# Performance work log

Measured on AMD Instinct MI355X. Metric: run time of the kernel, lower is better.

## Reference

```python
import jax, jax.numpy as jnp
import numpy as np

N = 100000   # nodes
E = 800000   # edges (avg degree 8)
D = 128      # input_dim == output_dim
H = 4        # num_heads
DH = D // H  # head_dim = 32


def setup_inputs() -> dict:
    key = jax.random.key(0)
    ks = jax.random.split(key, 12)
    s = 1.0 / np.sqrt(D)
    x = jax.random.normal(ks[0], (N, D), jnp.float32)
    row = jnp.sort(jax.random.randint(ks[1], (E,), 0, N))  # destination (query) nodes
    col = jax.random.randint(ks[2], (E,), 0, N)            # source (key/value) nodes
    Wq = jax.random.normal(ks[3], (D, D), jnp.float32) * s
    bq = jax.random.normal(ks[4], (D,), jnp.float32) * 0.01
    Wk = jax.random.normal(ks[5], (D, D), jnp.float32) * s
    bk = jax.random.normal(ks[6], (D,), jnp.float32) * 0.01
    Wv = jax.random.normal(ks[7], (D, D), jnp.float32) * s
    bv = jax.random.normal(ks[8], (D,), jnp.float32) * 0.01
    Wo = jax.random.normal(ks[9], (D, D), jnp.float32) * s
    bo = jax.random.normal(ks[10], (D,), jnp.float32) * 0.01
    return {"x": x, "row": row, "col": col, "Wq": Wq, "bq": bq, "Wk": Wk,
            "bk": bk, "Wv": Wv, "bv": bv, "Wo": Wo, "bo": bo}


def reference(x, row, col, Wq, bq, Wk, bk, Wv, bv, Wo, bo):
    n = x.shape[0]
    # projections; reshape (N, head_dim, num_heads) exactly as the torch code
    # NOTE: source scales q by k.size(-1)**0.5 == sqrt(num_heads) (quirk, kept faithful)
    scale = jnp.asarray(H, x.dtype) ** 0.5
    q = ((x @ Wq.T + bq).reshape(n, DH, H)) / scale
    k = (x @ Wk.T + bk).reshape(n, DH, H)
    v = (x @ Wv.T + bv).reshape(n, DH, H)
    # bsddmm: per-edge, per-head scores s[e,h] = q[row[e],:,h] . k[col[e],:,h]
    s = jnp.einsum('edh,edh->eh', q[row], k[col])  # (E, H)
    # sparse row-wise softmax over incoming edges of each destination node
    m = jax.ops.segment_max(s, row, num_segments=n)      # (N, H)
    e = jnp.exp(s - m[row])                               # (E, H)
    z = jax.ops.segment_sum(e, row, num_segments=n)      # (N, H)
    a = e / z[row]                                        # (E, H) attention weights
    # bspmm: y[i,:,h] = sum_{e: row[e]=i} a[e,h] * v[col[e],:,h]
    y = jax.ops.segment_sum(a[:, None, :] * v[col], row, num_segments=n)  # (N, DH, H)
    return y.reshape(n, D) @ Wo.T + bo
```

## Files before the change

kernel.cpp:

```cpp
#include <hip/hip_runtime.h>
#include <hip/hip_bf16.h>
#include <hip/hip_fp16.h>
#include <math.h>

#define D 128
#define H 4

typedef __attribute__((ext_vector_type(8))) short bf16x8;
typedef __attribute__((ext_vector_type(4))) float f32x4;

__device__ __forceinline__ unsigned short f32_to_bf16_rne(float f) {
    union { float f; unsigned u; } c; c.f = f;
    unsigned u = c.u;
    return (unsigned short)((u + 0x7FFFu + ((u >> 16) & 1u)) >> 16);
}
__device__ __forceinline__ float bf16_to_f32(unsigned short h) {
    union { unsigned u; float f; } c; c.u = ((unsigned)h) << 16;
    return c.f;
}

__device__ __forceinline__ void split_store(const float4 f0, const float4 f1,
                                            unsigned short* dh, unsigned short* dl)
{
    float fa[8] = {f0.x, f0.y, f0.z, f0.w, f1.x, f1.y, f1.z, f1.w};
    union { bf16x8 v; unsigned short s[8]; } hv, lv;
#pragma unroll
    for (int j = 0; j < 8; ++j) {
        unsigned short hh = f32_to_bf16_rne(fa[j]);
        hv.s[j] = hh;
        lv.s[j] = f32_to_bf16_rne(fa[j] - bf16_to_f32(hh));
    }
    *(bf16x8*)dh = hv.v;
    *(bf16x8*)dl = lv.v;
}

__global__ __launch_bounds__(256) void convert_w(
    const float* __restrict__ Wq, const float* __restrict__ Wk,
    const float* __restrict__ Wv, const float* __restrict__ Wo,
    unsigned short* __restrict__ wh, unsigned short* __restrict__ wl)
{
    int i = blockIdx.x * blockDim.x + threadIdx.x;
    if (i >= D * D) return;
    int r = i >> 7;
    int c = i & 127;
    int pr = ((r & 3) << 5) | (r >> 2);
    int pc = ((c & 3) << 5) | (c >> 2);
    const float* Ws[4] = {Wq, Wk, Wv, Wo};
#pragma unroll
    for (int m = 0; m < 4; ++m) {
        float f = Ws[m][i];
        unsigned short h = f32_to_bf16_rne(f);
        unsigned short l = f32_to_bf16_rne(f - bf16_to_f32(h));
        int dst = (m < 3) ? (pr * D + c) : (r * D + pc);
        wh[m * D * D + dst] = h;
        wl[m * D * D + dst] = l;
    }
}

#define RT 64

__global__ __launch_bounds__(512) void gemm_pipe(
    const float* __restrict__ A,
    const unsigned short* __restrict__ whAll, const unsigned short* __restrict__ wlAll,
    const float* __restrict__ b0, const float* __restrict__ b1,
    const float* __restrict__ b2,
    void* __restrict__ o0, void* __restrict__ o1, void* __restrict__ o2,
    float scale0, int n, int wbase, int halfmask, int permBias,
    int nsel, int gx)
{
    __shared__ unsigned short Ah[2][RT * 128];
    __shared__ unsigned short Al[2][RT * 128];

    const int sel    = blockIdx.x % nsel;
    const int tile0  = blockIdx.x / nsel;
    const int tstride = gridDim.x / nsel;

    const unsigned short* wh = whAll + (size_t)(wbase + sel) * D * D;
    const unsigned short* wl = wlAll + (size_t)(wbase + sel) * D * D;
    const float* bias = (sel == 0) ? b0 : (sel == 1 ? b1 : b2);
    void* out        = (sel == 0) ? o0 : (sel == 1 ? o1 : o2);
    const float scale = (sel == 0) ? scale0 : 1.0f;
    const bool halfOut = (halfmask >> sel) & 1;

    const int wid  = threadIdx.x >> 6;
    const int lane = threadIdx.x & 63;
    const int quad = lane >> 4;
    const int l16  = lane & 15;

    const unsigned short* wrh = wh + (size_t)(wid * 16 + l16) * D + quad * 8;
    const unsigned short* wrl = wl + (size_t)(wid * 16 + l16) * D + quad * 8;
    bf16x8 bh[4], bl[4];
#pragma unroll
    for (int kc = 0; kc < 4; ++kc) {
        bh[kc] = *(const bf16x8*)(wrh + kc * 32);
        bl[kc] = *(const bf16x8*)(wrl + kc * 32);
    }

    const int idxA = threadIdx.x;
    const int idxB = threadIdx.x + 512;
    const int rA = idxA >> 4, cA = idxA & 15;
    const int rB = idxB >> 4, cB = idxB & 15;
    const int dA = rA * 128 + ((cA ^ (rA & 15)) * 8);
    const int dB = rB * 128 + ((cB ^ (rB & 15)) * 8);

    {
        int rgA = tile0 * RT + rA; if (rgA > n - 1) rgA = n - 1;
        int rgB = tile0 * RT + rB; if (rgB > n - 1) rgB = n - 1;
        const float4* pA = (const float4*)(A + (size_t)rgA * D + cA * 8);
        const float4* pB = (const float4*)(A + (size_t)rgB * D + cB * 8);
        float4 a0 = pA[0], a1 = pA[1], a2 = pB[0], a3 = pB[1];
        split_store(a0, a1, &Ah[0][dA], &Al[0][dA]);
        split_store(a2, a3, &Ah[0][dB], &Al[0][dB]);
    }
    __syncthreads();

    int cur = 0;
    for (int t = tile0; t < gx; t += tstride) {
        const int tn = t + tstride;
        const bool more = (tn < gx);

        float4 a0, a1, a2, a3;
        if (more) {
            int rgA = tn * RT + rA; if (rgA > n - 1) rgA = n - 1;
            int rgB = tn * RT + rB; if (rgB > n - 1) rgB = n - 1;
            const float4* pA = (const float4*)(A + (size_t)rgA * D + cA * 8);
            const float4* pB = (const float4*)(A + (size_t)rgB * D + cB * 8);
            a0 = pA[0]; a1 = pA[1]; a2 = pB[0]; a3 = pB[1];
        }

        f32x4 acc[4];
#pragma unroll
        for (int rt = 0; rt < 4; ++rt) acc[rt] = (f32x4){0.f, 0.f, 0.f, 0.f};

#pragma unroll
        for (int kc = 0; kc < 4; ++kc) {
            const int cs = ((quad + 4 * kc) ^ l16) * 8;
            bf16x8 ah[4], al[4];
#pragma unroll
            for (int rt = 0; rt < 4; ++rt) {
                const int r = rt * 16 + l16;
                ah[rt] = *(const bf16x8*)&Ah[cur][r * 128 + cs];
                al[rt] = *(const bf16x8*)&Al[cur][r * 128 + cs];
            }
#pragma unroll
            for (int rt = 0; rt < 4; ++rt)
                acc[rt] = __builtin_amdgcn_mfma_f32_16x16x32_bf16(ah[rt], bh[kc], acc[rt], 0, 0, 0);
#pragma unroll
            for (int rt = 0; rt < 4; ++rt)
                acc[rt] = __builtin_amdgcn_mfma_f32_16x16x32_bf16(al[rt], bh[kc], acc[rt], 0, 0, 0);
#pragma unroll
            for (int rt = 0; rt < 4; ++rt)
                acc[rt] = __builtin_amdgcn_mfma_f32_16x16x32_bf16(ah[rt], bl[kc], acc[rt], 0, 0, 0);
        }

        const int m0 = t * RT;
        const int colg = wid * 16 + l16;
        const int bidx = permBias ? (((colg & 31) << 2) | (colg >> 5)) : colg;
        const float bv = bias[bidx];
        if (halfOut) {
            __half* oph = (__half*)out;
#pragma unroll
            for (int rt = 0; rt < 4; ++rt) {
#pragma unroll
                for (int r = 0; r < 4; ++r) {
                    int rowg = m0 + rt * 16 + quad * 4 + r;
                    if (rowg < n)
                        oph[(size_t)rowg * D + colg] = __float2half(acc[rt][r] + bv);
                }
            }
        } else {
            float* opf = (float*)out;
#pragma unroll
            for (int rt = 0; rt < 4; ++rt) {
#pragma unroll
                for (int r = 0; r < 4; ++r) {
                    int rowg = m0 + rt * 16 + quad * 4 + r;
                    if (rowg < n)
                        opf[(size_t)rowg * D + colg] = (acc[rt][r] + bv) * scale;
                }
            }
        }

        if (more) {
            split_store(a0, a1, &Ah[cur ^ 1][dA], &Al[cur ^ 1][dA]);
            split_store(a2, a3, &Ah[cur ^ 1][dB], &Al[cur ^ 1][dB]);
        }
        __syncthreads();
        cur ^= 1;
    }
}

__global__ void build_row_start(const int* __restrict__ row,
                                int* __restrict__ row_start, int n, int e)
{
    int i = blockIdx.x * blockDim.x + threadIdx.x;
    if (i > n) return;
    int lo = 0, hi = e;
    while (lo < hi) {
        int mid = (lo + hi) >> 1;
        if (row[mid] < i) lo = mid + 1; else hi = mid;
    }
    row_start[i] = lo;
}

#define MAXDEG 64
#define WPB 4

template<bool BIG>
__device__ __forceinline__ void edge_loop(
    int lane, int sub, int grp, int deg, int e0,
    const int* cmrow, const int* __restrict__ col,
    const float4 qa, const float4 qb,
    const __half* __restrict__ k, const __half* __restrict__ v,
    float& acc0, float& acc1, float& z)
{
    for (int e = 0; e < deg; e += 4) {
        const int ei = e + grp;
        int c0, c1, c2, c3, cs;
        if (!BIG) {
            const int4 cc = *(const int4*)&cmrow[e];
            c0 = cc.x; c1 = cc.y; c2 = cc.z; c3 = cc.w;
            cs = cmrow[ei < deg ? ei : deg - 1];
        } else {
            int es = ei < deg ? ei : deg - 1;
            cs = col[e0 + es];
            int e1 = e + 1 < deg ? e + 1 : deg - 1;
            int e2 = e + 2 < deg ? e + 2 : deg - 1;
            int e3 = e + 3 < deg ? e + 3 : deg - 1;
            c0 = col[e0 + e];
            c1 = col[e0 + e1];
            c2 = col[e0 + e2];
            c3 = col[e0 + e3];
        }
        __half2 v0 = ((const __half2*)(v + ((size_t)c0 << 7)))[lane];
        __half2 v1 = ((const __half2*)(v + ((size_t)c1 << 7)))[lane];
        __half2 v2 = ((const __half2*)(v + ((size_t)c2 << 7)))[lane];
        __half2 v3 = ((const __half2*)(v + ((size_t)c3 << 7)))[lane];
        union { bf16x8 v8; __half hx[8]; } ku;
        ku.v8 = *(const bf16x8*)(k + ((size_t)cs << 7) + sub * 8);
        float p = qa.x * __half2float(ku.hx[0]) + qa.y * __half2float(ku.hx[1])
                + qa.z * __half2float(ku.hx[2]) + qa.w * __half2float(ku.hx[3])
                + qb.x * __half2float(ku.hx[4]) + qb.y * __half2float(ku.hx[5])
                + qb.z * __half2float(ku.hx[6]) + qb.w * __half2float(ku.hx[7]);
        p += __shfl_xor(p, 1);
        p += __shfl_xor(p, 2);
        float ep = (ei < deg) ? __expf(p) : 0.f;
        float a0 = __shfl(ep,      4 * grp);
        float a1 = __shfl(ep, 16 + 4 * grp);
        float a2 = __shfl(ep, 32 + 4 * grp);
        float a3 = __shfl(ep, 48 + 4 * grp);
        z += (a0 + a1) + (a2 + a3);
        acc0 += a0 * __half2float(v0.x) + a1 * __half2float(v1.x)
              + a2 * __half2float(v2.x) + a3 * __half2float(v3.x);
        acc1 += a0 * __half2float(v0.y) + a1 * __half2float(v1.y)
              + a2 * __half2float(v2.y) + a3 * __half2float(v3.y);
    }
}

__global__ __launch_bounds__(WPB * 64) void edge_attn(
    const int* __restrict__ row_start,
    const float* __restrict__ q, const __half* __restrict__ k,
    const __half* __restrict__ v, const int* __restrict__ col,
    float* __restrict__ y, int n)
{
    __shared__ int cm[WPB][MAXDEG];

    const int wid  = threadIdx.x >> 6;
    const int lane = threadIdx.x & 63;
    const int node = blockIdx.x * WPB + wid;
    if (node >= n) return;

    const int e0  = row_start[node];
    const int deg = row_start[node + 1] - e0;
    const int sub = lane & 15;
    const int grp = lane >> 4;

    const float4* q4 = (const float4*)(q + (size_t)node * D) + sub * 2;
    const float4 qa = q4[0], qb = q4[1];

    float acc0 = 0.f, acc1 = 0.f, z = 0.f;

    if (deg <= MAXDEG) {
        const int dl4 = (deg + 3) & ~3;
        for (int i = lane; i < dl4; i += 64) {
            int ii = i < deg ? i : deg - 1;
            cm[wid][i] = col[e0 + ii];
        }
        edge_loop<false>(lane, sub, grp, deg, e0, cm[wid], col, qa, qb, k, v,
                         acc0, acc1, z);
    } else {
        edge_loop<true>(lane, sub, grp, deg, e0, cm[wid], col, qa, qb, k, v,
                        acc0, acc1, z);
    }

    const float rz = (z > 0.f) ? 1.f / z : 0.f;
    acc0 *= rz;
    acc1 *= rz;

    float2 o; o.x = acc0; o.y = acc1;
    ((float2*)y)[(size_t)node * 64 + lane] = o;
}

extern "C" void kernel_launch(void* const* d_in, const int* in_sizes, int n_in,
                              void* d_out, int out_size, void* d_ws, size_t ws_size,
                              hipStream_t stream)
{
    const float* x   = (const float*)d_in[0];
    const int*   row = (const int*)  d_in[1];
    const int*   col = (const int*)  d_in[2];
    const float* Wq  = (const float*)d_in[3];
    const float* bq  = (const float*)d_in[4];
    const float* Wk  = (const float*)d_in[5];
    const float* bk  = (const float*)d_in[6];
    const float* Wv  = (const float*)d_in[7];
    const float* bv  = (const float*)d_in[8];
    const float* Wo  = (const float*)d_in[9];
    const float* bo  = (const float*)d_in[10];
    float* out = (float*)d_out;

    const int n = in_sizes[0] / D;
    const int e = in_sizes[1];
    const size_t ND = (size_t)n * D;

    float* ws = (float*)d_ws;
    float*  q  = ws;
    __half* kh = (__half*)(ws + ND);
    __half* vh = kh + ND;
    float*  y  = ws + 2 * ND;
    unsigned short* wh = (unsigned short*)(ws + 3 * ND);
    unsigned short* wl = wh + 4 * D * D;
    int* row_start = (int*)(wl + 4 * D * D);

    const int gx = (n + RT - 1) / RT;

    convert_w<<<(D * D + 255) / 256, 256, 0, stream>>>(Wq, Wk, Wv, Wo, wh, wl);

    gemm_pipe<<<510, 512, 0, stream>>>(
        x, wh, wl, bq, bk, bv,
        (void*)q, (void*)kh, (void*)vh, 0.5f, n, 0, 6, 1,
        3, gx);

    build_row_start<<<(n + 1 + 255) / 256, 256, 0, stream>>>(row, row_start, n, e);

    edge_attn<<<(n + WPB - 1) / WPB, WPB * 64, 0, stream>>>(
        row_start, q, kh, vh, col, y, n);

    gemm_pipe<<<512, 512, 0, stream>>>(
        y, wh, wl, bo, bo, bo,
        (void*)out, (void*)out, (void*)out, 1.0f, n, 3, 0, 0,
        1, gx);
}
```

Measured before the change: 261.3 us.

## Fuse edge attention with output projection via per-block LDS tile and MFMA

Edge attention and the output projection now run in one kernel. Each 256-thread block processes 32 nodes, four waves of eight nodes each, and stages the attention outputs in shared memory. It then multiplies that tile by Wo with split-bf16 MFMA (hi*hi + lo*hi + hi*lo) and adds the bias. This removes the y intermediate round-trip through global memory and one kernel launch. The cost is that each block reloads Wo slices from global or L2, and occupancy may drop because each wave handles eight nodes serially.

```diff
diff --git a/kernel.cpp b/kernel.cpp
--- a/kernel.cpp
+++ b/kernel.cpp
@@ -19,8 +19,8 @@
     return c.f;
 }
 
-__device__ __forceinline__ void split_store(const float4 f0, const float4 f1,
-                                            unsigned short* dh, unsigned short* dl)
+__device__ __forceinline__ void split8(const float4 f0, const float4 f1,
+                                       bf16x8& hout, bf16x8& lout)
 {
     float fa[8] = {f0.x, f0.y, f0.z, f0.w, f1.x, f1.y, f1.z, f1.w};
     union { bf16x8 v; unsigned short s[8]; } hv, lv;
@@ -30,8 +30,17 @@
         hv.s[j] = hh;
         lv.s[j] = f32_to_bf16_rne(fa[j] - bf16_to_f32(hh));
     }
-    *(bf16x8*)dh = hv.v;
-    *(bf16x8*)dl = lv.v;
+    hout = hv.v;
+    lout = lv.v;
+}
+
+__device__ __forceinline__ void split_store(const float4 f0, const float4 f1,
+                                            unsigned short* dh, unsigned short* dl)
+{
+    bf16x8 h, l;
+    split8(f0, f1, h, l);
+    *(bf16x8*)dh = h;
+    *(bf16x8*)dl = l;
 }
 
 __global__ __launch_bounds__(256) void convert_w(
@@ -204,7 +213,8 @@
 }
 
 #define MAXDEG 64
-#define WPB 4
+#define NPB 32
+#define YLD 132
 
 template<bool BIG>
 __device__ __forceinline__ void edge_loop(
@@ -257,48 +267,99 @@
     }
 }
 
-__global__ __launch_bounds__(WPB * 64) void edge_attn(
+__global__ __launch_bounds__(256) void edge_oproj(
     const int* __restrict__ row_start,
     const float* __restrict__ q, const __half* __restrict__ k,
     const __half* __restrict__ v, const int* __restrict__ col,
-    float* __restrict__ y, int n)
-{
-    __shared__ int cm[WPB][MAXDEG];
+    const unsigned short* __restrict__ whAll, const unsigned short* __restrict__ wlAll,
+    const float* __restrict__ bo, float* __restrict__ out, int n)
+{
+    __shared__ float Y[NPB * YLD];
+    __shared__ int   cm[4][MAXDEG];
 
     const int wid  = threadIdx.x >> 6;
     const int lane = threadIdx.x & 63;
-    const int node = blockIdx.x * WPB + wid;
-    if (node >= n) return;
-
-    const int e0  = row_start[node];
-    const int deg = row_start[node + 1] - e0;
-    const int sub = lane & 15;
-    const int grp = lane >> 4;
-
-    const float4* q4 = (const float4*)(q + (size_t)node * D) + sub * 2;
-    const float4 qa = q4[0], qb = q4[1];
-
-    float acc0 = 0.f, acc1 = 0.f, z = 0.f;
-
-    if (deg <= MAXDEG) {
-        const int dl4 = (deg + 3) & ~3;
-        for (int i = lane; i < dl4; i += 64) {
-            int ii = i < deg ? i : deg - 1;
-            cm[wid][i] = col[e0 + ii];
-        }
-        edge_loop<false>(lane, sub, grp, deg, e0, cm[wid], col, qa, qb, k, v,
-                         acc0, acc1, z);
-    } else {
-        edge_loop<true>(lane, sub, grp, deg, e0, cm[wid], col, qa, qb, k, v,
-                        acc0, acc1, z);
-    }
-
-    const float rz = (z > 0.f) ? 1.f / z : 0.f;
-    acc0 *= rz;
-    acc1 *= rz;
-
-    float2 o; o.x = acc0; o.y = acc1;
-    ((float2*)y)[(size_t)node * 64 + lane] = o;
+    const int quad = lane >> 4;
+    const int l16  = lane & 15;
+    const int base = blockIdx.x * NPB;
+
+    for (int i = 0; i < 8; ++i) {
+        const int lr   = wid * 8 + i;
+        const int node = base + lr;
+        float acc0 = 0.f, acc1 = 0.f, z = 0.f;
+        if (node < n) {
+            const int e0  = row_start[node];
+            const int deg = row_start[node + 1] - e0;
+            const float4* q4 = (const float4*)(q + (size_t)node * D) + l16 * 2;
+            const float4 qa = q4[0], qb = q4[1];
+            if (deg <= MAXDEG) {
+                const int dl4 = (deg + 3) & ~3;
+                for (int ii = lane; ii < dl4; ii += 64) {
+                    int jj = ii < deg ? ii : deg - 1;
+                    cm[wid][ii] = col[e0 + jj];
+                }
+                edge_loop<false>(lane, l16, quad, deg, e0, cm[wid], col,
+                                 qa, qb, k, v, acc0, acc1, z);
+            } else {
+                edge_loop<true>(lane, l16, quad, deg, e0, cm[wid], col,
+                                qa, qb, k, v, acc0, acc1, z);
+            }
+        }
+        const float rz = (z > 0.f) ? 1.f / z : 0.f;
+        float2 o; o.x = acc0 * rz; o.y = acc1 * rz;
+        *(float2*)&Y[lr * YLD + 2 * lane] = o;
+    }
+    __syncthreads();
+
+    const unsigned short* wh = whAll + (size_t)3 * D * D;
+    const unsigned short* wl = wlAll + (size_t)3 * D * D;
+
+#pragma unroll 1
+    for (int s = 0; s < 2; ++s) {
+        const int colg = wid * 32 + s * 16 + l16;
+        const unsigned short* wrh = wh + (size_t)colg * D + quad * 8;
+        const unsigned short* wrl = wl + (size_t)colg * D + quad * 8;
+        bf16x8 bh[4], bl[4];
+#pragma unroll
+        for (int kc = 0; kc < 4; ++kc) {
+            bh[kc] = *(const bf16x8*)(wrh + kc * 32);
+            bl[kc] = *(const bf16x8*)(wrl + kc * 32);
+        }
+
+        f32x4 a0 = (f32x4){0.f, 0.f, 0.f, 0.f};
+        f32x4 a1 = (f32x4){0.f, 0.f, 0.f, 0.f};
+#pragma unroll
+        for (int kc = 0; kc < 4; ++kc) {
+            const int kb = quad * 8 + kc * 32;
+            const float4 f00 = *(const float4*)&Y[(l16)      * YLD + kb];
+            const float4 f01 = *(const float4*)&Y[(l16)      * YLD + kb + 4];
+            const float4 f10 = *(const float4*)&Y[(16 + l16) * YLD + kb];
+            const float4 f11 = *(const float4*)&Y[(16 + l16) * YLD + kb + 4];
+            bf16x8 ah0, al0, ah1, al1;
+            split8(f00, f01, ah0, al0);
+            split8(f10, f11, ah1, al1);
+            a0 = __builtin_amdgcn_mfma_f32_16x16x32_bf16(ah0, bh[kc], a0, 0, 0, 0);
+            a1 = __builtin_amdgcn_mfma_f32_16x16x32_bf16(ah1, bh[kc], a1, 0, 0, 0);
+            a0 = __builtin_amdgcn_mfma_f32_16x16x32_bf16(al0, bh[kc], a0, 0, 0, 0);
+            a1 = __builtin_amdgcn_mfma_f32_16x16x32_bf16(al1, bh[kc], a1, 0, 0, 0);
+            a0 = __builtin_amdgcn_mfma_f32_16x16x32_bf16(ah0, bl[kc], a0, 0, 0, 0);
+            a1 = __builtin_amdgcn_mfma_f32_16x16x32_bf16(ah1, bl[kc], a1, 0, 0, 0);
+        }
+
+        const float bv = bo[colg];
+#pragma unroll
+        for (int r = 0; r < 4; ++r) {
+            int rowg = base + quad * 4 + r;
+            if (rowg < n)
+                out[(size_t)rowg * D + colg] = a0[r] + bv;
+        }
+#pragma unroll
+        for (int r = 0; r < 4; ++r) {
+            int rowg = base + 16 + quad * 4 + r;
+            if (rowg < n)
+                out[(size_t)rowg * D + colg] = a1[r] + bv;
+        }
+    }
 }
 
 extern "C" void kernel_launch(void* const* d_in, const int* in_sizes, int n_in,
@@ -326,8 +387,7 @@
     float*  q  = ws;
     __half* kh = (__half*)(ws + ND);
     __half* vh = kh + ND;
-    float*  y  = ws + 2 * ND;
-    unsigned short* wh = (unsigned short*)(ws + 3 * ND);
+    unsigned short* wh = (unsigned short*)(ws + 2 * ND);
     unsigned short* wl = wh + 4 * D * D;
     int* row_start = (int*)(wl + 4 * D * D);
 
@@ -342,11 +402,6 @@
 
     build_row_start<<<(n + 1 + 255) / 256, 256, 0, stream>>>(row, row_start, n, e);
 
-    edge_attn<<<(n + WPB - 1) / WPB, WPB * 64, 0, stream>>>(
-        row_start, q, kh, vh, col, y, n);
-
-    gemm_pipe<<<512, 512, 0, stream>>>(
-        y, wh, wl, bo, bo, bo,
-        (void*)out, (void*)out, (void*)out, 1.0f, n, 3, 0, 0,
-        1, gx);
-}
+    edge_oproj<<<(n + NPB - 1) / NPB, 256, 0, stream>>>(
+        row_start, q, kh, vh, col, wh, wl, bo, out, n);
+}
```

Measured after the change: 301.3 us. +15.3%, slower.
